# Optimization experiments

Measured on AMD Instinct MI355X. Metric: run time of the kernel, lower is better.

The kernel has to match this reference:

```python
import jax, jax.numpy as jnp
import numpy as np

B, L, M, N, C = 2, 1024, 8, 16, 16
H, W, D = 64, 64, 16  # d == c: one histogram plane per feature channel


def setup_inputs() -> dict:
    key = jax.random.key(0)
    k1, k2, k3, k4, k5 = jax.random.split(key, 5)
    feats_src_dst = jax.random.normal(k1, (B, L, N, C), dtype=jnp.float32)
    voxels_src = jax.random.randint(k2, (B, L, 2), 0, 64).astype(jnp.int32)
    voxels_dst = jax.random.randint(k3, (B, L, 2), 0, 64).astype(jnp.int32)
    idxs_src = jax.random.randint(k4, (B, L, M), 0, L).astype(jnp.int32)
    idxs_dst = jax.random.randint(k5, (B, L, N), 0, L).astype(jnp.int32)
    return {
        "feats_src_dst": feats_src_dst,
        "voxels_src": voxels_src,
        "voxels_dst": voxels_dst,
        "idxs_src": idxs_src,
        "idxs_dst": idxs_dst,
    }


def reference(feats_src_dst, voxels_src, voxels_dst, idxs_src, idxs_dst):
    b, l, m = idxs_src.shape
    n = idxs_dst.shape[-1]
    c = feats_src_dst.shape[-1]
    dt = feats_src_dst.dtype

    gather = jax.vmap(lambda arr, idx: arr[idx])  # per-batch fancy gather

    s = idxs_src                                   # [b,l,m]  src KNN of each anchor
    dd = gather(idxs_dst, s)                       # [b,l,m,n] dst KNN of each src neighbor
    vsrc = gather(voxels_src.astype(dt), s)        # [b,l,m,2]
    vdst = gather(voxels_dst.astype(dt), dd)       # [b,l,m,n,2]
    wf = gather(feats_src_dst, s)                  # [b,l,m,n,c] vote weights

    # translation -> centered histogram bin
    t = vdst - vsrc[:, :, :, None, :]              # [b,l,m,n,2] (y,x)
    by = jnp.floor(t[..., 0]).astype(jnp.int32) + H // 2
    bx = jnp.floor(t[..., 1]).astype(jnp.int32) + W // 2
    valid = (by >= 0) & (by < H) & (bx >= 0) & (bx < W)
    by = jnp.clip(by, 0, H - 1)
    bx = jnp.clip(bx, 0, W - 1)
    wf = jnp.where(valid[..., None], wf, jnp.zeros((), dt))

    bi = jnp.broadcast_to(jnp.arange(b)[:, None, None, None], (b, l, m, n))
    li = jnp.broadcast_to(jnp.arange(l)[None, :, None, None], (b, l, m, n))

    hist = jnp.zeros((b, l, H, W, c), dt)
    hist = hist.at[bi, li, by, bx].add(wf)         # scatter-add voting
    return jnp.transpose(hist, (0, 1, 4, 2, 3))    # [b,l,c,h,w]
```

## Files before the change

### kernel.cpp

```cpp
#include <hip/hip_runtime.h>

#define B_ 2
#define L_ 1024
#define M_ 8
#define N_ 16
#define C_ 16
#define H_ 64
#define W_ 64

#define NVOTE (M_ * N_)
#define PLANE (H_ * W_)

__global__ __launch_bounds__(256) void hough_vote_plane_kernel(
    const float* __restrict__ feats,
    const int*   __restrict__ voxels_src,
    const int*   __restrict__ voxels_dst,
    const int*   __restrict__ idxs_src,
    const int*   __restrict__ idxs_dst,
    float*       __restrict__ out)
{
    const int gb  = blockIdx.x;
    const int bl  = gb >> 4;
    const int c   = gb & (C_ - 1);
    const int b   = bl >> 10;
    const int tid = threadIdx.x;

    __shared__ float s_plane[PLANE];

    float w   = 0.f;
    int   bin = -1;
    if (tid < NVOTE) {
        int m    = tid >> 4;
        int n    = tid & (N_ - 1);
        int s    = idxs_src[bl * M_ + m];
        int base = b * L_ + s;
        int2 vs  = ((const int2*)voxels_src)[base];
        int  dd  = idxs_dst[base * N_ + n];
        int2 vd  = ((const int2*)voxels_dst)[b * L_ + dd];
        int by = vd.x - vs.x + H_ / 2;
        int bx = vd.y - vs.y + W_ / 2;
        if (by >= 0 && by < H_ && bx >= 0 && bx < W_) {
            bin = by * W_ + bx;
            w   = feats[((size_t)base * N_ + n) * C_ + c];
        }
    }

    float4* p4 = (float4*)s_plane;
    #pragma unroll
    for (int i = 0; i < PLANE / 4 / 256; ++i)
        p4[i * 256 + tid] = make_float4(0.f, 0.f, 0.f, 0.f);
    __syncthreads();

    if (bin >= 0) atomicAdd(&s_plane[bin], w);
    __syncthreads();

    float4* o4 = (float4*)(out + ((size_t)bl * C_ + c) * PLANE);
    #pragma unroll
    for (int i = 0; i < PLANE / 4 / 256; ++i)
        o4[i * 256 + tid] = p4[i * 256 + tid];
}

extern "C" void kernel_launch(void* const* d_in, const int* in_sizes, int n_in,
                              void* d_out, int out_size, void* d_ws, size_t ws_size,
                              hipStream_t stream) {
    const float* feats      = (const float*)d_in[0];
    const int*   voxels_src = (const int*)d_in[1];
    const int*   voxels_dst = (const int*)d_in[2];
    const int*   idxs_src   = (const int*)d_in[3];
    const int*   idxs_dst   = (const int*)d_in[4];
    float*       out        = (float*)d_out;

    hough_vote_plane_kernel<<<B_ * L_ * C_, 256, 0, stream>>>(
        feats, voxels_src, voxels_dst, idxs_src, idxs_dst, out);
}
```

Baseline: 527.2 us.

## Split vote precompute into separate kernel and use nontemporal output stores

Adds a precompute kernel that computes each vote's bin and gathers its 16 feature weights once per (b,l), writing them to workspace in a channel-major layout. The plane kernel then reads only coalesced bin and weight data instead of redoing the dependent index gathers for every channel. Output planes are written with nontemporal stores to avoid polluting cache. This costs an extra launch and a workspace round trip, and the output write (about 537 MB) likely still dominates.

Measured after the change: 534.0 us. No clear change (+1.3%).

```diff
diff --git a/kernel.cpp b/kernel.cpp
--- a/kernel.cpp
+++ b/kernel.cpp
@@ -11,53 +11,79 @@
 #define NVOTE (M_ * N_)
 #define PLANE (H_ * W_)
 
-__global__ __launch_bounds__(256) void hough_vote_plane_kernel(
+typedef float vfloat4 __attribute__((ext_vector_type(4)));
+
+
+__global__ __launch_bounds__(128) void vote_precompute(
     const float* __restrict__ feats,
     const int*   __restrict__ voxels_src,
     const int*   __restrict__ voxels_dst,
     const int*   __restrict__ idxs_src,
     const int*   __restrict__ idxs_dst,
+    int*         __restrict__ ws_bin,
+    float*       __restrict__ ws_w)
+{
+    const int bl = blockIdx.x;
+    const int b  = bl >> 10;
+    const int t  = threadIdx.x;
+    const int m  = t >> 4;
+    const int n  = t & (N_ - 1);
+
+    int  s    = idxs_src[bl * M_ + m];
+    int  base = b * L_ + s;
+    int2 vs   = ((const int2*)voxels_src)[base];
+    int  dd   = idxs_dst[base * N_ + n];
+    int2 vd   = ((const int2*)voxels_dst)[b * L_ + dd];
+
+    int by = vd.x - vs.x + H_ / 2;
+    int bx = vd.y - vs.y + W_ / 2;
+    bool valid = (by >= 0) & (by < H_) & (bx >= 0) & (bx < W_);
+    ws_bin[bl * NVOTE + t] = valid ? (by * W_ + bx) : -1;
+
+    const vfloat4* f4 = (const vfloat4*)(feats + ((size_t)base * N_ + n) * C_);
+    vfloat4 w0 = f4[0], w1 = f4[1], w2 = f4[2], w3 = f4[3];
+    float wr[C_] = { w0.x, w0.y, w0.z, w0.w,  w1.x, w1.y, w1.z, w1.w,
+                     w2.x, w2.y, w2.z, w2.w,  w3.x, w3.y, w3.z, w3.w };
+
+    float* wb = ws_w + (size_t)bl * (C_ * NVOTE) + t;
+    #pragma unroll
+    for (int c = 0; c < C_; ++c)
+        wb[c * NVOTE] = wr[c];
+}
+
+__global__ __launch_bounds__(256) void hough_plane_kernel(
+    const int*   __restrict__ ws_bin,
+    const float* __restrict__ ws_w,
     float*       __restrict__ out)
 {
     const int gb  = blockIdx.x;
     const int bl  = gb >> 4;
     const int c   = gb & (C_ - 1);
-    const int b   = bl >> 10;
     const int tid = threadIdx.x;
 
     __shared__ float s_plane[PLANE];
 
+    int   bin = -1;
     float w   = 0.f;
-    int   bin = -1;
     if (tid < NVOTE) {
-        int m    = tid >> 4;
-        int n    = tid & (N_ - 1);
-        int s    = idxs_src[bl * M_ + m];
-        int base = b * L_ + s;
-        int2 vs  = ((const int2*)voxels_src)[base];
-        int  dd  = idxs_dst[base * N_ + n];
-        int2 vd  = ((const int2*)voxels_dst)[b * L_ + dd];
-        int by = vd.x - vs.x + H_ / 2;
-        int bx = vd.y - vs.y + W_ / 2;
-        if (by >= 0 && by < H_ && bx >= 0 && bx < W_) {
-            bin = by * W_ + bx;
-            w   = feats[((size_t)base * N_ + n) * C_ + c];
-        }
+        bin = ws_bin[bl * NVOTE + tid];
+        w   = ws_w[((size_t)bl * C_ + c) * NVOTE + tid];
     }
 
-    float4* p4 = (float4*)s_plane;
+    vfloat4* p4 = (vfloat4*)s_plane;
+    vfloat4  z  = {0.f, 0.f, 0.f, 0.f};
     #pragma unroll
     for (int i = 0; i < PLANE / 4 / 256; ++i)
-        p4[i * 256 + tid] = make_float4(0.f, 0.f, 0.f, 0.f);
+        p4[i * 256 + tid] = z;
     __syncthreads();
 
     if (bin >= 0) atomicAdd(&s_plane[bin], w);
     __syncthreads();
 
-    float4* o4 = (float4*)(out + ((size_t)bl * C_ + c) * PLANE);
+    vfloat4* o4 = (vfloat4*)(out + (size_t)gb * PLANE);
     #pragma unroll
     for (int i = 0; i < PLANE / 4 / 256; ++i)
-        o4[i * 256 + tid] = p4[i * 256 + tid];
+        __builtin_nontemporal_store(p4[i * 256 + tid], &o4[i * 256 + tid]);
 }
 
 extern "C" void kernel_launch(void* const* d_in, const int* in_sizes, int n_in,
@@ -70,6 +96,12 @@
     const int*   idxs_dst   = (const int*)d_in[4];
     float*       out        = (float*)d_out;
 
-    hough_vote_plane_kernel<<<B_ * L_ * C_, 256, 0, stream>>>(
-        feats, voxels_src, voxels_dst, idxs_src, idxs_dst, out);
+    int*   ws_bin = (int*)d_ws;
+    float* ws_w   = (float*)((char*)d_ws + (1 << 20));
+
+    vote_precompute<<<B_ * L_, 128, 0, stream>>>(
+        feats, voxels_src, voxels_dst, idxs_src, idxs_dst, ws_bin, ws_w);
+
+    hough_plane_kernel<<<B_ * L_ * C_, 256, 0, stream>>>(
+        ws_bin, ws_w, out);
 }
```
